# Performance work log

Measured on AMD Instinct MI355X. Metric: run time of the kernel, lower is better.

## Reference

```python
import jax, jax.numpy as jnp
import numpy as np

H = 256   # encoder/decoder hidden size
U = 128   # attention units


def setup_inputs() -> dict:
    key = jax.random.key(0)
    ks = jax.random.split(key, 8)
    B, Td, Te = 16, 128, 1024
    s = 1.0 / np.sqrt(H)
    return {
        "dec_outputs": jax.random.normal(ks[0], (B, Td, H), dtype=jnp.float32),
        "enc_outputs": jax.random.normal(ks[1], (B, Te, H), dtype=jnp.float32),
        "W1": jax.random.normal(ks[2], (H, U), dtype=jnp.float32) * s,
        "b1": jnp.zeros((U,), dtype=jnp.float32),
        "W2": jax.random.normal(ks[3], (H, U), dtype=jnp.float32) * s,
        "b2": jnp.zeros((U,), dtype=jnp.float32),
        "V": jax.random.normal(ks[4], (U, 1), dtype=jnp.float32) * (1.0 / np.sqrt(U)),
        "bv": jnp.zeros((1,), dtype=jnp.float32),
    }


def reference(dec_outputs, enc_outputs, W1, b1, W2, b2, V, bv):
    # Project once (the original redundantly re-projects enc_outputs per step).
    # w1d: [B, Td, U], w2e: [B, Te, U]
    w1d = jnp.einsum("bth,hu->btu", dec_outputs, W1) + b1
    w2e = jnp.einsum("bsh,hu->bsu", enc_outputs, W2) + b2
    # Additive Bahdanau score: tanh over broadcast sum -> [B, Td, Te, U]
    feat = jnp.tanh(w1d[:, :, None, :] + w2e[:, None, :, :])
    # V projection to scalar score: [B, Td, Te]
    score = jnp.einsum("btsu,u->bts", feat, V[:, 0]) + bv[0]
    # Softmax over encoder positions (original Softmax(axis=1) on [B, Te])
    return jax.nn.softmax(score, axis=-1)
```

## Files before the change

### kernel.cpp

```cpp
#include <hip/hip_runtime.h>
#include <math.h>

#define HB 256
#define UB 128
#define BB 16
#define TD 128
#define TE 1024

#define CLAMP_W 7.0f
#define L2E2 2.8853900817779268f
#define ALPHA 1.52587890625e-05f
#define NEG2ALPHA (-3.0517578125e-05f)

__device__ __forceinline__ float stage_exp(float w, float shift) {
    float t = fminf(fmaxf(w, -CLAMP_W), CLAMP_W);
    return exp2f(fmaf(t, L2E2, shift));
}

#define DEC_SLABS 32
#define ENC_SLABS 256
#define DEC_BLOCKS (16 * DEC_SLABS)
#define ENC_BLOCKS (16 * ENC_SLABS)

__global__ __launch_bounds__(64) void proj_v6(
    const float* __restrict__ dec, const float* __restrict__ enc,
    const float* __restrict__ W1, const float* __restrict__ b1,
    const float* __restrict__ W2, const float* __restrict__ b2,
    float* __restrict__ Ea, float* __restrict__ Eb) {
    const int blk = blockIdx.x;
    const bool is_dec = blk < DEC_BLOCKS;
    const int rel   = is_dec ? blk : blk - DEC_BLOCKS;
    const int nslab = is_dec ? DEC_SLABS : ENC_SLABS;
    const int ut    = rel / nslab;
    const int slab  = rel - ut * nslab;
    const float* __restrict__ X    = is_dec ? dec : enc;
    const float* __restrict__ W    = is_dec ? W1 : W2;
    const float* __restrict__ bias = is_dec ? b1 : b2;

    const int l = threadIdx.x;
    const long row = (long)slab * 64 + l;
    const float* xr = X + row * HB;
    const int u0 = ut * 8;

    float acc[8];
    #pragma unroll
    for (int j = 0; j < 8; ++j) acc[j] = 0.f;

    for (int h = 0; h < HB; h += 8) {
        float4 x0 = *reinterpret_cast<const float4*>(xr + h);
        float4 x1 = *reinterpret_cast<const float4*>(xr + h + 4);
        float4 w[8][2];
        #pragma unroll
        for (int k = 0; k < 8; ++k) {
            w[k][0] = *reinterpret_cast<const float4*>(W + (h + k) * UB + u0);
            w[k][1] = *reinterpret_cast<const float4*>(W + (h + k) * UB + u0 + 4);
        }
        const float xk[8] = {x0.x, x0.y, x0.z, x0.w, x1.x, x1.y, x1.z, x1.w};
        #pragma unroll
        for (int k = 0; k < 8; ++k) {
            acc[0] = fmaf(xk[k], w[k][0].x, acc[0]);
            acc[1] = fmaf(xk[k], w[k][0].y, acc[1]);
            acc[2] = fmaf(xk[k], w[k][0].z, acc[2]);
            acc[3] = fmaf(xk[k], w[k][0].w, acc[3]);
            acc[4] = fmaf(xk[k], w[k][1].x, acc[4]);
            acc[5] = fmaf(xk[k], w[k][1].y, acc[5]);
            acc[6] = fmaf(xk[k], w[k][1].z, acc[6]);
            acc[7] = fmaf(xk[k], w[k][1].w, acc[7]);
        }
    }

    float4 bv0 = *reinterpret_cast<const float4*>(bias + u0);
    float4 bv1 = *reinterpret_cast<const float4*>(bias + u0 + 4);
    const float sh = is_dec ? -16.f : 0.f;
    float4 q0 = make_float4(stage_exp(acc[0] + bv0.x, sh), stage_exp(acc[1] + bv0.y, sh),
                            stage_exp(acc[2] + bv0.z, sh), stage_exp(acc[3] + bv0.w, sh));
    float4 q1 = make_float4(stage_exp(acc[4] + bv1.x, sh), stage_exp(acc[5] + bv1.y, sh),
                            stage_exp(acc[6] + bv1.z, sh), stage_exp(acc[7] + bv1.w, sh));

    if (is_dec) {
        const long bq = row >> 7;
        const int  t  = (int)(row & (TD - 1));
        float4* dst = reinterpret_cast<float4*>(Ea);
        dst[(bq * 32 + ut * 2 + 0) * TD + t] = q0;
        dst[(bq * 32 + ut * 2 + 1) * TD + t] = q1;
    } else {
        const long bq = row >> 10;
        const int  s  = (int)(row & (TE - 1));
        float4* dst = reinterpret_cast<float4*>(Eb);
        dst[(bq * 32 + ut * 2 + 0) * TE + s] = q0;
        dst[(bq * 32 + ut * 2 + 1) * TE + s] = q1;
    }
}

__global__ __launch_bounds__(1024) void score_v6(
    const float* __restrict__ Ea4,
    const float4* __restrict__ Eb4,
    const float* __restrict__ V,
    float* __restrict__ out) {
    const int tid = threadIdx.x;
    const int wv = tid >> 6, l = tid & 63;
    const int i = blockIdx.x;
    const int b  = 2 * (i & 7) + ((i >> 3) >> 4);
    const int t0 = ((i >> 3) & 15) * 8;

    const float*  ab = Ea4 + ((long)b * 32 * TD) * 4;
    const float4* ep = Eb4 + (long)b * 32 * TE + tid;
    const float alphav = ALPHA;

    float acc[8];
    #pragma unroll
    for (int t = 0; t < 8; ++t) acc[t] = 0.f;

#define SCSTREAM(U4, E) do {                                              \
        const float* _a = ab + ((long)(U4) * TD + t0) * 4;                \
        float4 _v = *reinterpret_cast<const float4*>(V + (U4) * 4);       \
        _Pragma("unroll")                                                 \
        for (int t = 0; t < 8; ++t) {                                     \
            float4 a4 = *reinterpret_cast<const float4*>(_a + t * 4);     \
            float X0 = fmaf(a4.x, (E).x, alphav);                         \
            float X1 = fmaf(a4.y, (E).y, alphav);                         \
            float X2 = fmaf(a4.z, (E).z, alphav);                         \
            float X3 = fmaf(a4.w, (E).w, alphav);                         \
            float P01 = X0 * X1, P23 = X2 * X3;                           \
            float N01 = fmaf(_v.x, X1, _v.y * X0);                        \
            float N23 = fmaf(_v.z, X3, _v.w * X2);                        \
            float N   = fmaf(N01, P23, N23 * P01);                        \
            acc[t] = fmaf(N, __builtin_amdgcn_rcpf(P01 * P23), acc[t]);   \
        }                                                                 \
    } while (0)

    #pragma unroll 2
    for (int u4 = 0; u4 < 16; ++u4) {
        float4 e0 = ep[(long)u4 * TE];
        float4 e1 = ep[(long)(u4 + 16) * TE];
        SCSTREAM(u4, e0);
        SCSTREAM(u4 + 16, e1);
    }
#undef SCSTREAM

    float sc[8];
    #pragma unroll
    for (int t = 0; t < 8; ++t) sc[t] = NEG2ALPHA * acc[t];

    __shared__ float red[8][16];
    #pragma unroll
    for (int t = 0; t < 8; ++t) {
        float x = sc[t];
        #pragma unroll
        for (int off = 32; off > 0; off >>= 1) x = fmaxf(x, __shfl_xor(x, off, 64));
        if (l == 0) red[t][wv] = x;
    }
    __syncthreads();
    float m[8];
    #pragma unroll
    for (int t = 0; t < 8; ++t) {
        float x = red[t][0];
        #pragma unroll
        for (int k = 1; k < 16; ++k) x = fmaxf(x, red[t][k]);
        m[t] = x;
    }
    __syncthreads();
    #pragma unroll
    for (int t = 0; t < 8; ++t) {
        sc[t] = __expf(sc[t] - m[t]);
        float x = sc[t];
        #pragma unroll
        for (int off = 32; off > 0; off >>= 1) x += __shfl_xor(x, off, 64);
        if (l == 0) red[t][wv] = x;
    }
    __syncthreads();
    #pragma unroll
    for (int t = 0; t < 8; ++t) {
        float x = red[t][0];
        #pragma unroll
        for (int k = 1; k < 16; ++k) x += red[t][k];
        out[((long)b * TD + t0 + t) * TE + tid] = sc[t] * (1.f / x);
    }
}

extern "C" void kernel_launch(void* const* d_in, const int* in_sizes, int n_in,
                              void* d_out, int out_size, void* d_ws, size_t ws_size,
                              hipStream_t stream) {
    const float* dec = (const float*)d_in[0];
    const float* enc = (const float*)d_in[1];
    const float* W1  = (const float*)d_in[2];
    const float* b1  = (const float*)d_in[3];
    const float* W2  = (const float*)d_in[4];
    const float* b2  = (const float*)d_in[5];
    const float* V   = (const float*)d_in[6];
    float* out = (float*)d_out;

    float* Ea = (float*)d_ws;
    float* Eb = Ea + (long)BB * 32 * TD * 4;

    proj_v6<<<DEC_BLOCKS + ENC_BLOCKS, 64, 0, stream>>>(dec, enc, W1, b1, W2, b2, Ea, Eb);
    score_v6<<<256, 1024, 0, stream>>>(Ea, (const float4*)Eb, V, out);
}
```

Baseline: 75.15 us.

## Restructure score kernel to register-cache decoder rows and split softmax into separate pass

Projection outputs are now stored row-major [B,T,U] through a shared-memory transpose instead of the u4-interleaved layout. The score kernel keeps each thread's decoder projection row in registers and loops over 8 encoder positions, so every decoder value is reused across several positions. Raw scores are written through a shared transpose, and a new third kernel runs a per-row softmax in place. This adds a full extra write and read of the score matrix plus a kernel launch, in exchange for better operand reuse in the tanh-sum stage.

Measured after the change: 202.4 us. 169% more time.

```diff
diff --git a/kernel.cpp b/kernel.cpp
--- a/kernel.cpp
+++ b/kernel.cpp
@@ -22,7 +22,7 @@
 #define DEC_BLOCKS (16 * DEC_SLABS)
 #define ENC_BLOCKS (16 * ENC_SLABS)
 
-__global__ __launch_bounds__(64) void proj_v6(
+__global__ __launch_bounds__(64) void proj_v7(
     const float* __restrict__ dec, const float* __restrict__ enc,
     const float* __restrict__ W1, const float* __restrict__ b1,
     const float* __restrict__ W2, const float* __restrict__ b2,
@@ -36,6 +36,7 @@
     const float* __restrict__ X    = is_dec ? dec : enc;
     const float* __restrict__ W    = is_dec ? W1 : W2;
     const float* __restrict__ bias = is_dec ? b1 : b2;
+    float* __restrict__ dst        = is_dec ? Ea : Eb;
 
     const int l = threadIdx.x;
     const long row = (long)slab * 64 + l;
@@ -69,113 +70,113 @@
         }
     }
 
-    float4 bv0 = *reinterpret_cast<const float4*>(bias + u0);
-    float4 bv1 = *reinterpret_cast<const float4*>(bias + u0 + 4);
     const float sh = is_dec ? -16.f : 0.f;
-    float4 q0 = make_float4(stage_exp(acc[0] + bv0.x, sh), stage_exp(acc[1] + bv0.y, sh),
-                            stage_exp(acc[2] + bv0.z, sh), stage_exp(acc[3] + bv0.w, sh));
-    float4 q1 = make_float4(stage_exp(acc[4] + bv1.x, sh), stage_exp(acc[5] + bv1.y, sh),
-                            stage_exp(acc[6] + bv1.z, sh), stage_exp(acc[7] + bv1.w, sh));
-
-    if (is_dec) {
-        const long bq = row >> 7;
-        const int  t  = (int)(row & (TD - 1));
-        float4* dst = reinterpret_cast<float4*>(Ea);
-        dst[(bq * 32 + ut * 2 + 0) * TD + t] = q0;
-        dst[(bq * 32 + ut * 2 + 1) * TD + t] = q1;
-    } else {
-        const long bq = row >> 10;
-        const int  s  = (int)(row & (TE - 1));
-        float4* dst = reinterpret_cast<float4*>(Eb);
-        dst[(bq * 32 + ut * 2 + 0) * TE + s] = q0;
-        dst[(bq * 32 + ut * 2 + 1) * TE + s] = q1;
+    __shared__ float tr[64][9];
+    #pragma unroll
+    for (int j = 0; j < 8; ++j)
+        tr[l][j] = stage_exp(acc[j] + bias[u0 + j], sh);
+    __syncthreads();
+
+    const int uj = l & 7, rj = l >> 3;
+    const long slabbase = (long)slab * 64;
+    #pragma unroll
+    for (int it = 0; it < 8; ++it) {
+        const int r = it * 8 + rj;
+        dst[(slabbase + r) * UB + u0 + uj] = tr[r][uj];
     }
 }
 
-__global__ __launch_bounds__(1024) void score_v6(
-    const float* __restrict__ Ea4,
-    const float4* __restrict__ Eb4,
+__global__ __launch_bounds__(512) void score_v7(
+    const float* __restrict__ Ea,
+    const float* __restrict__ Eb,
     const float* __restrict__ V,
-    float* __restrict__ out) {
+    float* __restrict__ outraw) {
+    const int tid = threadIdx.x;
+    const int lane = tid & 63;
+    const int wave = __builtin_amdgcn_readfirstlane(tid >> 6);
+    const int pair = wave >> 1;
+    const int t = (wave & 1) * 64 + lane;
+    const int i = blockIdx.x;
+    const int b  = 2 * (i & 7) + ((i >> 3) >> 5);
+    const int sc0 = ((i >> 3) & 31) * 32;
+    const int s0 = sc0 + pair * 8;
+
+    const float* __restrict__ ap = Ea + ((long)b * TD + t) * UB;
+    const float* __restrict__ ebase = Eb + ((long)b * TE + s0) * UB;
+    const float alphav = ALPHA;
+
+    float acc[8];
+    #pragma unroll
+    for (int ss = 0; ss < 8; ++ss) acc[ss] = 0.f;
+
+    #pragma unroll
+    for (int half = 0; half < 2; ++half) {
+        float4 a[16];
+        #pragma unroll
+        for (int k = 0; k < 16; ++k)
+            a[k] = *reinterpret_cast<const float4*>(ap + half * 64 + k * 4);
+        const float* __restrict__ vp = V + half * 64;
+
+        #pragma unroll
+        for (int ss = 0; ss < 8; ++ss) {
+            const float* __restrict__ ep = ebase + ss * UB + half * 64;
+            float a8 = 0.f;
+            #pragma unroll 4
+            for (int u4 = 0; u4 < 16; ++u4) {
+                float4 e = *reinterpret_cast<const float4*>(ep + u4 * 4);
+                float4 v = *reinterpret_cast<const float4*>(vp + u4 * 4);
+                float4 A = a[u4];
+                float X0 = fmaf(A.x, e.x, alphav);
+                float X1 = fmaf(A.y, e.y, alphav);
+                float X2 = fmaf(A.z, e.z, alphav);
+                float X3 = fmaf(A.w, e.w, alphav);
+                float P01 = X0 * X1, P23 = X2 * X3;
+                float N01 = fmaf(v.x, X1, v.y * X0);
+                float N23 = fmaf(v.z, X3, v.w * X2);
+                float N   = fmaf(N01, P23, N23 * P01);
+                a8 = fmaf(N, __builtin_amdgcn_rcpf(P01 * P23), a8);
+            }
+            acc[ss] += a8;
+        }
+    }
+
+    __shared__ float tr[128][33];
+    #pragma unroll
+    for (int ss = 0; ss < 8; ++ss) tr[t][pair * 8 + ss] = NEG2ALPHA * acc[ss];
+    __syncthreads();
+    const int r  = tid >> 2;
+    const int c0 = (tid & 3) * 8;
+    float* orow = outraw + ((long)b * TD + r) * TE + sc0 + c0;
+    #pragma unroll
+    for (int k = 0; k < 8; ++k) orow[k] = tr[r][c0 + k];
+}
+
+__global__ __launch_bounds__(1024) void softmax_v7(float* __restrict__ out) {
+    const long row = blockIdx.x;
+    float* p = out + row * TE;
     const int tid = threadIdx.x;
     const int wv = tid >> 6, l = tid & 63;
-    const int i = blockIdx.x;
-    const int b  = 2 * (i & 7) + ((i >> 3) >> 4);
-    const int t0 = ((i >> 3) & 15) * 8;
-
-    const float*  ab = Ea4 + ((long)b * 32 * TD) * 4;
-    const float4* ep = Eb4 + (long)b * 32 * TE + tid;
-    const float alphav = ALPHA;
-
-    float acc[8];
-    #pragma unroll
-    for (int t = 0; t < 8; ++t) acc[t] = 0.f;
-
-#define SCSTREAM(U4, E) do {                                              \
-        const float* _a = ab + ((long)(U4) * TD + t0) * 4;                \
-        float4 _v = *reinterpret_cast<const float4*>(V + (U4) * 4);       \
-        _Pragma("unroll")                                                 \
-        for (int t = 0; t < 8; ++t) {                                     \
-            float4 a4 = *reinterpret_cast<const float4*>(_a + t * 4);     \
-            float X0 = fmaf(a4.x, (E).x, alphav);                         \
-            float X1 = fmaf(a4.y, (E).y, alphav);                         \
-            float X2 = fmaf(a4.z, (E).z, alphav);                         \
-            float X3 = fmaf(a4.w, (E).w, alphav);                         \
-            float P01 = X0 * X1, P23 = X2 * X3;                           \
-            float N01 = fmaf(_v.x, X1, _v.y * X0);                        \
-            float N23 = fmaf(_v.z, X3, _v.w * X2);                        \
-            float N   = fmaf(N01, P23, N23 * P01);                        \
-            acc[t] = fmaf(N, __builtin_amdgcn_rcpf(P01 * P23), acc[t]);   \
-        }                                                                 \
-    } while (0)
-
-    #pragma unroll 2
-    for (int u4 = 0; u4 < 16; ++u4) {
-        float4 e0 = ep[(long)u4 * TE];
-        float4 e1 = ep[(long)(u4 + 16) * TE];
-        SCSTREAM(u4, e0);
-        SCSTREAM(u4 + 16, e1);
-    }
-#undef SCSTREAM
-
-    float sc[8];
-    #pragma unroll
-    for (int t = 0; t < 8; ++t) sc[t] = NEG2ALPHA * acc[t];
-
-    __shared__ float red[8][16];
-    #pragma unroll
-    for (int t = 0; t < 8; ++t) {
-        float x = sc[t];
-        #pragma unroll
-        for (int off = 32; off > 0; off >>= 1) x = fmaxf(x, __shfl_xor(x, off, 64));
-        if (l == 0) red[t][wv] = x;
-    }
-    __syncthreads();
-    float m[8];
-    #pragma unroll
-    for (int t = 0; t < 8; ++t) {
-        float x = red[t][0];
-        #pragma unroll
-        for (int k = 1; k < 16; ++k) x = fmaxf(x, red[t][k]);
-        m[t] = x;
-    }
-    __syncthreads();
-    #pragma unroll
-    for (int t = 0; t < 8; ++t) {
-        sc[t] = __expf(sc[t] - m[t]);
-        float x = sc[t];
-        #pragma unroll
-        for (int off = 32; off > 0; off >>= 1) x += __shfl_xor(x, off, 64);
-        if (l == 0) red[t][wv] = x;
-    }
-    __syncthreads();
-    #pragma unroll
-    for (int t = 0; t < 8; ++t) {
-        float x = red[t][0];
-        #pragma unroll
-        for (int k = 1; k < 16; ++k) x += red[t][k];
-        out[((long)b * TD + t0 + t) * TE + tid] = sc[t] * (1.f / x);
-    }
+
+    float x = p[tid];
+    __shared__ float red[16];
+    float m = x;
+    #pragma unroll
+    for (int off = 32; off > 0; off >>= 1) m = fmaxf(m, __shfl_xor(m, off, 64));
+    if (l == 0) red[wv] = m;
+    __syncthreads();
+    #pragma unroll
+    for (int k = 0; k < 16; ++k) m = fmaxf(m, red[k]);
+    __syncthreads();
+    float e = __expf(x - m);
+    float s = e;
+    #pragma unroll
+    for (int off = 32; off > 0; off >>= 1) s += __shfl_xor(s, off, 64);
+    if (l == 0) red[wv] = s;
+    __syncthreads();
+    s = 0.f;
+    #pragma unroll
+    for (int k = 0; k < 16; ++k) s += red[k];
+    p[tid] = e * (1.f / s);
 }
 
 extern "C" void kernel_launch(void* const* d_in, const int* in_sizes, int n_in,
@@ -191,8 +192,9 @@
     float* out = (float*)d_out;
 
     float* Ea = (float*)d_ws;
-    float* Eb = Ea + (long)BB * 32 * TD * 4;
-
-    proj_v6<<<DEC_BLOCKS + ENC_BLOCKS, 64, 0, stream>>>(dec, enc, W1, b1, W2, b2, Ea, Eb);
-    score_v6<<<256, 1024, 0, stream>>>(Ea, (const float4*)Eb, V, out);
-}
+    float* Eb = Ea + (long)BB * TD * UB;
+
+    proj_v7<<<DEC_BLOCKS + ENC_BLOCKS, 64, 0, stream>>>(dec, enc, W1, b1, W2, b2, Ea, Eb);
+    score_v7<<<512, 512, 0, stream>>>(Ea, Eb, V, out);
+    softmax_v7<<<BB * TD, 1024, 0, stream>>>(out);
+}
```
